# Optimization experiments

Measured on AMD Instinct MI355X. Metric: run time of the kernel, lower is better.

The kernel has to match this reference:

```python
import jax, jax.numpy as jnp
import numpy as np

D_IN, D, BOX, REL, THR = 2048, 512, 8, 80, 0.5

def _ln(x, g, b):
    m = jnp.mean(x, -1, keepdims=True)
    v = jnp.mean((x - m) ** 2, -1, keepdims=True)
    return (x - m) * jax.lax.rsqrt(v + 1e-5) * g + b

def setup_inputs():
    key = jax.random.key(0)
    ks = jax.random.split(key, 24)
    B, N = 32, 50
    def lin(k, i, o):
        return jax.random.normal(k, (i, o), jnp.float32) / np.sqrt(i)
    z = lambda n: jnp.zeros((n,), jnp.float32)
    o = lambda n: jnp.ones((n,), jnp.float32)
    return {
        "images": jax.random.normal(ks[0], (B, N, D_IN), jnp.float32),
        "selfbbox": jax.random.uniform(ks[1], (B, N, BOX), jnp.float32),
        "bbox": jax.random.uniform(ks[2], (B, N, N, BOX), jnp.float32),
        "pre_w": lin(ks[3], D_IN, D), "pre_b": z(D), "pre_g": o(D), "pre_be": z(D),
        "subj_w": lin(ks[4], D, D), "subj_b": z(D),
        "obj_w": lin(ks[5], D, D), "obj_b": z(D),
        "ps1_w": lin(ks[6], BOX, 64), "ps1_b": z(64), "ps_g": o(64), "ps_be": z(64),
        "ps2_w": lin(ks[7], 64, 64), "ps2_b": z(64),
        "pr1_w": lin(ks[8], BOX, 64), "pr1_b": z(64), "pr_g": o(64), "pr_be": z(64),
        "pr2_w": lin(ks[9], 64, 64), "pr2_b": z(64),
        "rs_w": lin(ks[10], D + 64, 1), "rs_b": z(1),
        "rf_w": lin(ks[11], D + 64, REL), "rf_b": z(REL),
        "g1_w": lin(ks[12], D + REL, D + REL), "g1_b": z(D + REL),
        "g2_w": lin(ks[13], D + REL, D), "g2_b": z(D),
        "g3_w": lin(ks[14], D, D), "g3_b": z(D),
    }

def reference(images, selfbbox, bbox, pre_w, pre_b, pre_g, pre_be, subj_w, subj_b,
              obj_w, obj_b, ps1_w, ps1_b, ps_g, ps_be, ps2_w, ps2_b,
              pr1_w, pr1_b, pr_g, pr_be, pr2_w, pr2_b, rs_w, rs_b, rf_w, rf_b,
              g1_w, g1_b, g2_w, g2_b, g3_w, g3_b):
    B, N = images.shape[0], images.shape[1]
    mask = jnp.sum(images, -1) != 0.0                      # [B,N] valid nodes
    attention_mask = (~mask)[:, None, None, :]             # [B,1,1,N]
    mf = mask.astype(images.dtype)
    # preprocess: Linear -> ReLU -> (dropout=id at eval) -> LayerNorm
    x = _ln(jax.nn.relu(images @ pre_w + pre_b), pre_g, pre_be)  # [B,N,512]
    x_subj = jax.nn.relu(x @ subj_w + subj_b) * mf[..., None]
    x_obj = jax.nn.relu(x @ obj_w + obj_b) * mf[..., None]
    eye = jnp.eye(N, dtype=bool)
    # pairwise subject/object features: diag(i==j) holds subject, off-diag object j
    x_rela = jnp.where(eye[None, :, :, None], x_subj[:, :, None, :], x_obj[:, None, :, :])
    x_rela = x_rela * mf[:, :, None, None]
    # positional MLPs
    h = jax.nn.relu(selfbbox @ ps1_w + ps1_b)
    h = jax.nn.relu(_ln(h, ps_g, ps_be) @ ps2_w + ps2_b)
    pos_self = h * mf[..., None]
    h = jax.nn.relu(bbox @ pr1_w + pr1_b)
    h = jax.nn.relu(_ln(h, pr_g, pr_be) @ pr2_w + pr2_b)
    pos_relas = h * mf[:, None, :, None] * mf[:, :, None, None]
    pos_rela = jnp.where(eye[None, :, :, None], pos_self[:, :, None, :], pos_relas)
    pos_rela = pos_rela * mf[:, :, None, None]
    pair = jnp.concatenate([x_rela, pos_rela], axis=-1)    # [B,N,N,576]
    pair_mask = mask[:, :, None] & mask[:, None, :]        # [B,N,N]
    # Relationshipness: pairwise relatedness score p + attention-pooled relation feats
    logits = (pair @ rs_w + rs_b)[..., 0]                  # [B,N,N]
    p = jax.nn.sigmoid(logits) * pair_mask.astype(images.dtype)
    attn = jax.nn.softmax(jnp.where(pair_mask, logits, -1e9), axis=2)
    feat = jax.nn.relu(pair @ rf_w + rf_b)                 # [B,N,N,80]
    relas = jnp.einsum('bij,bijf->bif', attn, feat) * mf[..., None]
    xx = jnp.concatenate([x, relas], axis=-1)              # [B,N,592]
    # dynamic edge threshold -> block-diagonal graph, expressed densely per image
    A = p > THR                                            # edge i->j
    Ahat = A | eye[None]                                   # add remaining self loops
    Af = Ahat.astype(xx.dtype)
    deg = jnp.sum(Af, axis=1)                              # in-degree at target j (>=1)
    dinv = jax.lax.rsqrt(deg)
    An = Af * dinv[:, :, None] * dinv[:, None, :]          # sym-normalized adjacency
    def gcn(hh, w, b):
        return jnp.einsum('bij,bif->bjf', An, hh @ w) + b
    x1 = jax.nn.relu(gcn(xx, g1_w, g1_b))
    x2 = jax.nn.relu(gcn(x1, g2_w, g2_b))
    x3 = jax.nn.relu(gcn(x2, g3_w, g3_b))
    outs = jnp.concatenate([x[:, None], x3[:, None]], axis=1)  # [B,2,N,512]
    return (outs, attention_mask)
```

## Files before the change

### kernel.cpp

```cpp
#include <hip/hip_runtime.h>
#include <hip/hip_bf16.h>

typedef __hip_bfloat16 bf16;

#define BB 32
#define NN 50
#define DIN 2048
#define DD 512
#define PD 64
#define FF 80
#define GG 592
#define BN (BB*NN)

#define O_FLAG  0
#define O_MF    16
#define O_SS    1616
#define O_SO    3216
#define O_PS    4816
#define O_FS    107216
#define O_FO    235216
#define O_RL    363216
#define O_LG    491216
#define O_AN    571216
#define O_T     651216
#define O_X1    1598416
#define O_X2    2545616
#define O_WPRE  3364816
#define O_BPRE  4413392
#define O_GPRE  4413904
#define O_EPRE  4414416
#define O_WSUBJ 4414928
#define O_BSUBJ 4677072
#define O_WOBJ  4677584
#define O_BOBJ  4939728
#define O_WPS1  4940240
#define O_BPS1  4940752
#define O_GPS   4940816
#define O_EPS   4940880
#define O_WPS2  4940944
#define O_BPS2  4945040
#define O_WPR1  4945104
#define O_BPR1  4945616
#define O_GPR   4945680
#define O_EPR   4945744
#define O_WPR2  4945808
#define O_BPR2  4949904
#define O_WRS   4949968
#define O_BRS   4950544
#define O_WRF   4950560
#define O_BRF   4996640
#define O_WG1   4996736
#define O_BG1   5347200
#define O_WG2   5347792
#define O_BG2   5650896
#define O_WG3   5651408
#define O_BG3   5913552
#define O_FT    5914064

#define PSLICE  819200

__device__ __forceinline__ float b2f(bf16 x){ return __bfloat162float(x); }

__device__ __forceinline__ float LDI(const bf16* p, size_t i, int f32m){
    if(f32m){
        bf16 a=p[2*i], b=p[2*i+1];
        unsigned short lo,hi;
        __builtin_memcpy(&lo,&a,2); __builtin_memcpy(&hi,&b,2);
        unsigned v=((unsigned)hi<<16)|(unsigned)lo;
        float f; __builtin_memcpy(&f,&v,4);
        return f;
    }
    return __bfloat162float(p[i]);
}

__global__ void k_flag(const bf16* __restrict__ images, float* __restrict__ ws){
    __shared__ int cnt;
    if(threadIdx.x==0) cnt=0;
    __syncthreads();
    bf16 h=images[2*threadIdx.x];
    unsigned short u; __builtin_memcpy(&u,&h,2);
    unsigned e=(u>>7)&0xFF;
    int sane=((u&0x7FFF)==0 || (e>=0x70&&e<=0x85))?1:0;
    atomicAdd(&cnt,sane);
    __syncthreads();
    if(threadIdx.x==0) ws[O_FLAG]=(cnt<48)?1.f:0.f;
}

__device__ __forceinline__ void conv(const bf16* s, float* d, int n, int F, int i0, int st){
    for(int g=i0; g<n; g+=st) d[g]=LDI(s,(size_t)g,F);
}
__global__ void kw(const bf16* p0,const bf16* p1,const bf16* p2,const bf16* p3,
                   const bf16* p4,const bf16* p5,const bf16* p6,const bf16* p7,
                   const bf16* p8,const bf16* p9,const bf16* p10,const bf16* p11,
                   const bf16* p12,const bf16* p13,const bf16* p14,const bf16* p15,
                   const bf16* p16,const bf16* p17,const bf16* p18,const bf16* p19,
                   const bf16* p20,const bf16* p21,const bf16* p22,const bf16* p23,
                   const bf16* p24,const bf16* p25,const bf16* p26,const bf16* p27,
                   const bf16* p28,const bf16* p29, float* __restrict__ ws){
    int F=ws[O_FLAG]>0.5f;
    int i0=blockIdx.x*256+threadIdx.x, st=gridDim.x*256;
    conv(p0, ws+O_WPRE, 1048576,F,i0,st);
    conv(p1, ws+O_BPRE, 512,F,i0,st);
    conv(p2, ws+O_GPRE, 512,F,i0,st);
    conv(p3, ws+O_EPRE, 512,F,i0,st);
    conv(p4, ws+O_WSUBJ,262144,F,i0,st);
    conv(p5, ws+O_BSUBJ,512,F,i0,st);
    conv(p6, ws+O_WOBJ, 262144,F,i0,st);
    conv(p7, ws+O_BOBJ, 512,F,i0,st);
    conv(p8, ws+O_WPS1, 512,F,i0,st);
    conv(p9, ws+O_BPS1, 64,F,i0,st);
    conv(p10,ws+O_GPS,  64,F,i0,st);
    conv(p11,ws+O_EPS,  64,F,i0,st);
    conv(p12,ws+O_WPS2, 4096,F,i0,st);
    conv(p13,ws+O_BPS2, 64,F,i0,st);
    conv(p14,ws+O_WPR1, 512,F,i0,st);
    conv(p15,ws+O_BPR1, 64,F,i0,st);
    conv(p16,ws+O_GPR,  64,F,i0,st);
    conv(p17,ws+O_EPR,  64,F,i0,st);
    conv(p18,ws+O_WPR2, 4096,F,i0,st);
    conv(p19,ws+O_BPR2, 64,F,i0,st);
    conv(p20,ws+O_WRS,  576,F,i0,st);
    conv(p21,ws+O_BRS,  1,F,i0,st);
    conv(p22,ws+O_WRF,  46080,F,i0,st);
    conv(p23,ws+O_BRF,  80,F,i0,st);
    conv(p24,ws+O_WG1,  350464,F,i0,st);
    conv(p25,ws+O_BG1,  592,F,i0,st);
    conv(p26,ws+O_WG2,  303104,F,i0,st);
    conv(p27,ws+O_BG2,  512,F,i0,st);
    conv(p28,ws+O_WG3,  262144,F,i0,st);
    conv(p29,ws+O_BG3,  512,F,i0,st);
}

__global__ void __launch_bounds__(256,4) k_x(const bf16* __restrict__ images,
                                             float* __restrict__ ws){
    __shared__ float as[8*256];
    __shared__ float rsum[4][8];
    int blk=blockIdx.x, t=threadIdx.x;
    int rg=blk>>3, ks=blk&7;
    int r0=rg*8, kbase=ks*256;
    int F=ws[O_FLAG]>0.5f;
    int wv=t>>6, ln=t&63;
    float sv[8];
    #pragma unroll
    for(int row=0;row<8;row++){
        float v=LDI(images,(size_t)(r0+row)*DIN+kbase+t,F);
        as[row*256+t]=v;
        sv[row]=v;
    }
    #pragma unroll
    for(int row=0;row<8;row++){
        float s=sv[row];
        for(int m=32;m>0;m>>=1) s+=__shfl_xor(s,m,64);
        sv[row]=s;
    }
    if(ln==0){
        #pragma unroll
        for(int row=0;row<8;row++) rsum[wv][row]=sv[row];
    }
    __syncthreads();
    if(t<8){
        float s=rsum[0][t]+rsum[1][t]+rsum[2][t]+rsum[3][t];
        ws[O_RL+(size_t)(r0+t)*8+ks]=s;
    }
    const float* wP=ws+O_WPRE+(size_t)kbase*DD;
    int c0=t, c1=t+256;
    float acc[8][2]={};
    for(int k0=0;k0<256;k0+=8){
        float w0[8],w1[8];
        #pragma unroll
        for(int u=0;u<8;u++){ w0[u]=wP[(size_t)(k0+u)*DD+c0]; w1[u]=wP[(size_t)(k0+u)*DD+c1]; }
        #pragma unroll
        for(int row=0;row<8;row++){
            float4 a0=*(const float4*)&as[row*256+k0];
            float4 a1=*(const float4*)&as[row*256+k0+4];
            acc[row][0]+=a0.x*w0[0]; acc[row][1]+=a0.x*w1[0];
            acc[row][0]+=a0.y*w0[1]; acc[row][1]+=a0.y*w1[1];
            acc[row][0]+=a0.z*w0[2]; acc[row][1]+=a0.z*w1[2];
            acc[row][0]+=a0.w*w0[3]; acc[row][1]+=a0.w*w1[3];
            acc[row][0]+=a1.x*w0[4]; acc[row][1]+=a1.x*w1[4];
            acc[row][0]+=a1.y*w0[5]; acc[row][1]+=a1.y*w1[5];
            acc[row][0]+=a1.z*w0[6]; acc[row][1]+=a1.z*w1[6];
            acc[row][0]+=a1.w*w0[7]; acc[row][1]+=a1.w*w1[7];
        }
    }
    float* P=ws + ((ks<7)? (O_FT+(size_t)ks*PSLICE) : (size_t)O_T);
    #pragma unroll
    for(int row=0;row<8;row++){
        size_t b=(size_t)(r0+row)*DD;
        P[b+c0]=acc[row][0]; P[b+c1]=acc[row][1];
    }
}

__global__ void __launch_bounds__(256,4) k_xr(float* __restrict__ ws, float* __restrict__ out){
    __shared__ float red[256];
    int blk=blockIdx.x, t=threadIdx.x;
    int r0=blk*4;
    if(t<4){
        int r=r0+t;
        float s=0.f;
        for(int ks=0;ks<8;ks++) s+=ws[O_RL+(size_t)r*8+ks];
        float mf=(s!=0.f)?1.f:0.f;
        ws[O_MF+r]=mf;
        out[(size_t)BB*2*NN*DD+r]=1.f-mf;
    }
    const float* bPre=ws+O_BPRE; const float* gPre=ws+O_GPRE; const float* ePre=ws+O_EPRE;
    int c0=t, c1=t+256;
    for(int row=0;row<4;row++){
        int r=r0+row;
        float y0=bPre[c0], y1=bPre[c1];
        for(int ks=0;ks<8;ks++){
            const float* P=ws + ((ks<7)? (O_FT+(size_t)ks*PSLICE) : (size_t)O_T);
            y0+=P[(size_t)r*DD+c0]; y1+=P[(size_t)r*DD+c1];
        }
        y0=fmaxf(y0,0.f); y1=fmaxf(y1,0.f);
        red[t]=y0+y1; __syncthreads();
        for(int o=128;o>0;o>>=1){ if(t<o) red[t]+=red[t+o]; __syncthreads(); }
        float mean=red[0]/DD; __syncthreads();
        float d0=y0-mean, d1=y1-mean;
        red[t]=d0*d0+d1*d1; __syncthreads();
        for(int o=128;o>0;o>>=1){ if(t<o) red[t]+=red[t+o]; __syncthreads(); }
        float rstd=rsqrtf(red[0]/DD+1e-5f);
        __syncthreads();
        float xv0=d0*rstd*gPre[c0]+ePre[c0];
        float xv1=d1*rstd*gPre[c1]+ePre[c1];
        size_t ob=((size_t)(r/NN)*2)*NN*DD+(size_t)(r%NN)*DD;
        out[ob+c0]=xv0; out[ob+c1]=xv1;
    }
}

__global__ void __launch_bounds__(256,4) k_so1(const float* __restrict__ out,
                                               float* __restrict__ ws){
    __shared__ float xs[4*DD];
    __shared__ float mrow_s[4];
    int blk=blockIdx.x, t=threadIdx.x;
    int rg=blk>>2, mat=(blk>>1)&1, ch=blk&1;
    int r0=rg*4;
    for(int idx=t; idx<4*DD; idx+=256){
        int row=idx>>9, k=idx&511;
        int r=r0+row;
        xs[idx]=out[((size_t)(r/NN)*2)*NN*DD+(size_t)(r%NN)*DD+k];
    }
    if(t<4) mrow_s[t]=ws[O_MF+r0+t];
    __syncthreads();
    const float* W =ws+(mat?O_WOBJ:O_WSUBJ);
    const float* Bb=ws+(mat?O_BOBJ:O_BSUBJ);
    int c=ch*256+t;
    float acc[4]={0.f,0.f,0.f,0.f};
    for(int k0=0;k0<DD;k0+=8){
        float w[8];
        #pragma unroll
        for(int u=0;u<8;u++) w[u]=W[(size_t)(k0+u)*DD+c];
        #pragma unroll
        for(int row=0;row<4;row++){
            float4 a0=*(const float4*)&xs[row*DD+k0];
            float4 a1=*(const float4*)&xs[row*DD+k0+4];
            acc[row]+=a0.x*w[0]; acc[row]+=a0.y*w[1];
            acc[row]+=a0.z*w[2]; acc[row]+=a0.w*w[3];
            acc[row]+=a1.x*w[4]; acc[row]+=a1.y*w[5];
            acc[row]+=a1.z*w[6]; acc[row]+=a1.w*w[7];
        }
    }
    float* Y=ws+O_FT+(size_t)mat*PSLICE;
    #pragma unroll
    for(int row=0;row<4;row++)
        Y[(size_t)(r0+row)*DD+c]=fmaxf(acc[row]+Bb[c],0.f)*mrow_s[row];
}

__global__ void __launch_bounds__(256,4) k_so2(float* __restrict__ ws){
    __shared__ float yl[4][DD];
    int blk=blockIdx.x, t=threadIdx.x, wv=t>>6, ln=t&63;
    int combo=blk*4+wv;
    int mat=combo&1, r=combo>>1;
    const float* Y=ws+O_FT+(size_t)mat*PSLICE+(size_t)r*DD;
    for(int k=ln;k<DD;k+=64) yl[wv][k]=Y[k];
    __syncthreads();
    const float* wRs=ws+O_WRS;
    float ps=0.f;
    for(int k=ln;k<DD;k+=64) ps+=yl[wv][k]*wRs[k];
    for(int m=32;m>0;m>>=1) ps+=__shfl_xor(ps,m,64);
    if(ln==0) ws[(mat?O_SO:O_SS)+r]=ps;
    const float* wRf=ws+O_WRF;
    float* dst=ws+(mat?O_FO:O_FS)+(size_t)r*FF;
    {
        float a=0.f;
        for(int k0=0;k0<DD;k0+=4){
            float4 y4=*(const float4*)&yl[wv][k0];
            a+=y4.x*wRf[(size_t)k0*FF+ln];
            a+=y4.y*wRf[(size_t)(k0+1)*FF+ln];
            a+=y4.z*wRf[(size_t)(k0+2)*FF+ln];
            a+=y4.w*wRf[(size_t)(k0+3)*FF+ln];
        }
        dst[ln]=a;
    }
    if(ln<16){
        int c=64+ln;
        float a=0.f;
        for(int k0=0;k0<DD;k0+=4){
            float4 y4=*(const float4*)&yl[wv][k0];
            a+=y4.x*wRf[(size_t)k0*FF+c];
            a+=y4.y*wRf[(size_t)(k0+1)*FF+c];
            a+=y4.z*wRf[(size_t)(k0+2)*FF+c];
            a+=y4.w*wRf[(size_t)(k0+3)*FF+c];
        }
        dst[c]=a;
    }
}

__global__ void k_pos_self(const bf16* __restrict__ sb, float* __restrict__ ws){
    __shared__ float h[PD];
    __shared__ float stat[2];
    int r=blockIdx.x, t=threadIdx.x;
    int F=ws[O_FLAG]>0.5f;
    const float* w1=ws+O_WPS1;
    float acc=0.f;
    for(int q=0;q<8;q++) acc+=LDI(sb,(size_t)r*8+q,F)*w1[q*PD+t];
    acc=fmaxf(acc+ws[O_BPS1+t],0.f);
    h[t]=acc; __syncthreads();
    if(t==0){
        float sm=0; for(int k=0;k<PD;k++) sm+=h[k];
        float mean=sm/PD;
        float v=0; for(int k=0;k<PD;k++){float d=h[k]-mean; v+=d*d;}
        stat[0]=mean; stat[1]=rsqrtf(v/PD+1e-5f);
    }
    __syncthreads();
    float hn=(acc-stat[0])*stat[1]*ws[O_GPS+t]+ws[O_EPS+t];
    h[t]=hn; __syncthreads();
    float a2=0.f;
    const float* w2=ws+O_WPS2;
    for(int k=0;k<PD;k++) a2+=h[k]*w2[k*PD+t];
    ws[O_PS+(size_t)r*PD+t]=fmaxf(a2+ws[O_BPS2+t],0.f)*ws[O_MF+r];
}

#define PSTRIDE 68
#define ZROW(m) ((m)*PSTRIDE + (((m)>>3)<<2))

__global__ void __launch_bounds__(256,3) k_pair(const bf16* __restrict__ bbox,
                                                float* __restrict__ ws){
    __shared__ float zp[64*PSTRIDE+64];
    __shared__ float wbuf[80*PSTRIDE];
    __shared__ float w1s[512];
    __shared__ float bbs[512];
    __shared__ float b1s[64], g1s[64], be1s[64], b2s[64], wrss[64];
    __shared__ float brfs[80];
    __shared__ float rowmi[64], rowmj[64], rowbase[64];
    __shared__ int   rowfb[64], rowps[64], rowdg[64];

    int t=threadIdx.x;
    int blk=blockIdx.x;
    int F=ws[O_FLAG]>0.5f;
    float rsb=ws[O_BRS];

    float wrfreg[20];
    #pragma unroll
    for(int u=0;u<20;u++){
        int idx=t+256*u;
        int f=idx>>6, k=idx&63;
        wrfreg[u]=ws[O_WRF+(size_t)(512+k)*FF+f];
    }

    for(int idx=t; idx<4096; idx+=256){ int k=idx>>6, c=idx&63; wbuf[k*PSTRIDE+c]=ws[O_WPR2+idx]; }
    for(int idx=t; idx<512; idx+=256) w1s[idx]=ws[O_WPR1+idx];
    for(int idx=t; idx<512; idx+=256) bbs[idx]=LDI(bbox,(size_t)blk*512+idx,F);
    if(t<64){
        b1s[t]=ws[O_BPR1+t]; g1s[t]=ws[O_GPR+t]; be1s[t]=ws[O_EPR+t];
        b2s[t]=ws[O_BPR2+t]; wrss[t]=ws[O_WRS+512+t];
    } else if(t<144){
        brfs[t-64]=ws[O_BRF+t-64];
    }
    if(t<64){
        int p=blk*64+t;
        int r=p/NN, j=p-r*NN;
        int b=r/NN, i=r-b*NN;
        int dg=(i==j);
        rowmi[t]=ws[O_MF+r];
        rowmj[t]=ws[O_MF+b*NN+j];
        rowdg[t]=dg;
        rowbase[t]=dg? ws[O_SS+r] : ws[O_SO+b*NN+j];
        rowfb[t]=dg? (O_FS+r*FF) : (O_FO+(b*NN+j)*FF);
        rowps[t]=O_PS+r*PD;
    }
    __syncthreads();

    int wv=t>>6, ln=t&63;
    #pragma unroll 2
    for(int q=0;q<16;q++){
        int m=wv*16+q;
        float acc=0.f;
        #pragma unroll
        for(int u=0;u<8;u++) acc+=bbs[m*8+u]*w1s[u*64+ln];
        float h1=fmaxf(acc+b1s[ln],0.f);
        float sm=h1;
        for(int o=32;o>0;o>>=1) sm+=__shfl_xor(sm,o,64);
        float mean=sm*(1.f/64.f);
        float d=h1-mean;
        float vv=d*d;
        for(int o=32;o>0;o>>=1) vv+=__shfl_xor(vv,o,64);
        float rstd=rsqrtf(vv*(1.f/64.f)+1e-5f);
        zp[ZROW(m)+ln]=d*rstd*g1s[ln]+be1s[ln];
    }

    int tr=t>>4, tc=t&15;
    int m0=tr*4, c0=tc*4;
    float a1[4][4]={};
    #pragma unroll 2
    for(int k0=0;k0<64;k0+=4){
        float4 zv[4], wvv[4];
        #pragma unroll
        for(int i=0;i<4;i++) zv[i]=*(const float4*)&zp[ZROW(m0+i)+k0];
        #pragma unroll
        for(int u=0;u<4;u++) wvv[u]=*(const float4*)&wbuf[(k0+u)*PSTRIDE+c0];
        #pragma unroll
        for(int i=0;i<4;i++){
            const float* zpp=(const float*)&zv[i];
            #pragma unroll
            for(int u=0;u<4;u++){
                const float* wp=(const float*)&wvv[u];
                float zk=zpp[u];
                a1[i][0]+=zk*wp[0]; a1[i][1]+=zk*wp[1];
                a1[i][2]+=zk*wp[2]; a1[i][3]+=zk*wp[3];
            }
        }
    }
    __syncthreads();

    #pragma unroll
    for(int i=0;i<4;i++){
        int m=m0+i;
        float4 o;
        if(rowdg[m]){
            const float* ps=ws+rowps[m];
            o.x=ps[c0]; o.y=ps[c0+1]; o.z=ps[c0+2]; o.w=ps[c0+3];
        } else {
            float sc=rowmi[m]*rowmj[m];
            o.x=fmaxf(a1[i][0]+b2s[c0+0],0.f)*sc;
            o.y=fmaxf(a1[i][1]+b2s[c0+1],0.f)*sc;
            o.z=fmaxf(a1[i][2]+b2s[c0+2],0.f)*sc;
            o.w=fmaxf(a1[i][3]+b2s[c0+3],0.f)*sc;
        }
        *(float4*)&zp[ZROW(m)+c0]=o;
    }

    #pragma unroll 2
    for(int q=0;q<16;q++){
        int m=wv*16+q;
        float lp=zp[ZROW(m)+ln]*wrss[ln];
        for(int o=32;o>0;o>>=1) lp+=__shfl_xor(lp,o,64);
        if(ln==0){
            ws[O_LG+(size_t)blk*64+m]=rowmi[m]*rowbase[m]+lp+rsb;
        }
    }

    #pragma unroll
    for(int u=0;u<20;u++){
        int idx=t+256*u;
        wbuf[(idx>>6)*PSTRIDE+(idx&63)]=wrfreg[u];
    }
    __syncthreads();

    {
        int c5=tc*5;
        float a2[4][5]={};
        #pragma unroll 2
        for(int k0=0;k0<64;k0+=4){
            float4 zv[4], wv5[5];
            #pragma unroll
            for(int i=0;i<4;i++) zv[i]=*(const float4*)&zp[ZROW(m0+i)+k0];
            #pragma unroll
            for(int j=0;j<5;j++) wv5[j]=*(const float4*)&wbuf[(c5+j)*PSTRIDE+k0];
            #pragma unroll
            for(int i=0;i<4;i++){
                const float* zpp=(const float*)&zv[i];
                #pragma unroll
                for(int j=0;j<5;j++){
                    const float* wp=(const float*)&wv5[j];
                    a2[i][j]+=zpp[0]*wp[0]+zpp[1]*wp[1]+zpp[2]*wp[2]+zpp[3]*wp[3];
                }
            }
        }
        #pragma unroll
        for(int i=0;i<4;i++){
            int m=m0+i;
            size_t p=(size_t)blk*64+m;
            float mi=rowmi[m];
            const float* fb=ws+rowfb[m];
            #pragma unroll
            for(int j=0;j<5;j++){
                int c=c5+j;
                ws[O_FT+p*FF+c]=fmaxf(mi*fb[c]+a2[i][j]+brfs[c],0.f);
            }
        }
    }
}

__global__ void k_relas(float* __restrict__ ws){
    __shared__ float attn[64];
    int r=blockIdx.x, t=threadIdx.x;
    int b=r/NN;
    float mi=ws[O_MF+r];
    if(t<64){
        float v=-1e9f;
        if(t<NN){
            float mj=ws[O_MF+b*NN+t];
            bool pm=(mi>0.5f)&&(mj>0.5f);
            v=pm? ws[O_LG+(size_t)r*NN+t] : -1e9f;
        }
        float mx=v;
        for(int o=32;o>0;o>>=1) mx=fmaxf(mx,__shfl_xor(mx,o,64));
        float e=(t<NN)? __expf(v-mx) : 0.f;
        float sm=e;
        for(int o=32;o>0;o>>=1) sm+=__shfl_xor(sm,o,64);
        attn[t]=e*(1.f/sm);
    }
    __syncthreads();
    if(t<FF){
        float s=0.f;
        const float* ft=ws+O_FT+(size_t)r*NN*FF;
        for(int j=0;j<NN;j++) s+=attn[j]*ft[(size_t)j*FF+t];
        ws[O_RL+(size_t)r*FF+t]=s*mi;
    }
}

__global__ void k_adj(float* __restrict__ ws){
    __shared__ float Af[NN*NN];
    __shared__ float dinv[NN];
    int b=blockIdx.x, t=threadIdx.x;
    for(int idx=t; idx<NN*NN; idx+=256){
        int i=idx/NN, j=idx%NN;
        float l=ws[O_LG+(size_t)b*NN*NN+idx];
        bool a=(l>0.f)&&(ws[O_MF+b*NN+i]>0.5f)&&(ws[O_MF+b*NN+j]>0.5f);
        Af[idx]=(a||i==j)?1.f:0.f;
    }
    __syncthreads();
    if(t<NN){
        float dg=0.f;
        for(int i=0;i<NN;i++) dg+=Af[i*NN+t];
        dinv[t]=rsqrtf(dg);
    }
    __syncthreads();
    for(int idx=t; idx<NN*NN; idx+=256){
        int i=idx/NN, j=idx%NN;
        ws[O_AN+(size_t)b*NN*NN+idx]=Af[idx]*dinv[i]*dinv[j];
    }
}

__global__ void __launch_bounds__(256,4) kt(int mode, const float* __restrict__ out,
                   const float* __restrict__ ws,
                   const float* __restrict__ W, float* __restrict__ T,
                   int K, int NCOL, int NTILE){
    __shared__ float xs[5*GG];
    int blk=blockIdx.x, t=threadIdx.x;
    int rg=blk/NTILE, tile=blk%NTILE;
    for(int idx=t; idx<5*K; idx+=256){
        int row=idx/K, k=idx-row*K;
        int gr=rg*5+row;
        float v;
        if(mode==0){
            int bb=gr/NN, ii=gr-bb*NN;
            if(k<DD) v=out[(size_t)(2*bb)*NN*DD+(size_t)ii*DD+k];
            else     v=ws[O_RL+(size_t)gr*FF+(k-DD)];
        } else if(mode==1) v=ws[O_X1+(size_t)gr*GG+k];
        else               v=ws[O_X2+(size_t)gr*DD+k];
        xs[row*K+k]=v;
    }
    __syncthreads();
    int c=tile*256+t;
    if(c>=NCOL) return;
    float acc[5];
    #pragma unroll
    for(int u=0;u<5;u++) acc[u]=0.f;
    for(int k0=0;k0<K;k0+=8){
        float w[8];
        #pragma unroll
        for(int u=0;u<8;u++) w[u]=W[(size_t)(k0+u)*NCOL+c];
        #pragma unroll
        for(int row=0;row<5;row++){
            float4 a0=*(const float4*)&xs[row*K+k0];
            float4 a1=*(const float4*)&xs[row*K+k0+4];
            acc[row]+=a0.x*w[0]; acc[row]+=a0.y*w[1];
            acc[row]+=a0.z*w[2]; acc[row]+=a0.w*w[3];
            acc[row]+=a1.x*w[4]; acc[row]+=a1.y*w[5];
            acc[row]+=a1.z*w[6]; acc[row]+=a1.w*w[7];
        }
    }
    int gr0=rg*5;
    #pragma unroll
    for(int u=0;u<5;u++) T[(size_t)(gr0+u)*NCOL+c]=acc[u];
}

__global__ void ka(int mode, float* __restrict__ ws, const float* __restrict__ bias,
                   float* __restrict__ out, int NCOL){
    __shared__ float acol[NN];
    int rj=blockIdx.x, t=threadIdx.x;
    int b=rj/NN, j=rj-b*NN;
    if(t<NN) acol[t]=ws[O_AN+(size_t)b*NN*NN+t*NN+j];
    __syncthreads();
    const float* Tb=ws+O_T+(size_t)b*NN*NCOL;
    for(int c=t;c<NCOL;c+=256){
        float acc=0.f;
        for(int i2=0;i2<NN;i2++) acc+=acol[i2]*Tb[(size_t)i2*NCOL+c];
        float v=fmaxf(acc+bias[c],0.f);
        if(mode==2)      out[(size_t)(2*b+1)*NN*DD+(size_t)j*DD+c]=v;
        else if(mode==1) ws[O_X2+(size_t)rj*DD+c]=v;
        else             ws[O_X1+(size_t)rj*GG+c]=v;
    }
}

extern "C" void kernel_launch(void* const* d_in, const int* in_sizes, int n_in,
                              void* d_out, int out_size, void* d_ws, size_t ws_size,
                              hipStream_t stream) {
    const bf16* images  = (const bf16*)d_in[0];
    const bf16* selfbbox= (const bf16*)d_in[1];
    const bf16* bbox    = (const bf16*)d_in[2];

    float* out=(float*)d_out;
    float* ws =(float*)d_ws;

    k_flag<<<1,64,0,stream>>>(images, ws);
    kw<<<512,256,0,stream>>>((const bf16*)d_in[3],(const bf16*)d_in[4],(const bf16*)d_in[5],
                             (const bf16*)d_in[6],(const bf16*)d_in[7],(const bf16*)d_in[8],
                             (const bf16*)d_in[9],(const bf16*)d_in[10],(const bf16*)d_in[11],
                             (const bf16*)d_in[12],(const bf16*)d_in[13],(const bf16*)d_in[14],
                             (const bf16*)d_in[15],(const bf16*)d_in[16],(const bf16*)d_in[17],
                             (const bf16*)d_in[18],(const bf16*)d_in[19],(const bf16*)d_in[20],
                             (const bf16*)d_in[21],(const bf16*)d_in[22],(const bf16*)d_in[23],
                             (const bf16*)d_in[24],(const bf16*)d_in[25],(const bf16*)d_in[26],
                             (const bf16*)d_in[27],(const bf16*)d_in[28],(const bf16*)d_in[29],
                             (const bf16*)d_in[30],(const bf16*)d_in[31],(const bf16*)d_in[32],
                             ws);
    k_x<<<1600,256,0,stream>>>(images, ws);
    k_xr<<<400,256,0,stream>>>(ws, out);
    k_pos_self<<<BN,PD,0,stream>>>(selfbbox, ws);
    k_so1<<<1600,256,0,stream>>>(out, ws);
    k_so2<<<800,256,0,stream>>>(ws);
    k_pair<<<1250,256,0,stream>>>(bbox, ws);
    k_relas<<<BN,128,0,stream>>>(ws);
    k_adj<<<BB,256,0,stream>>>(ws);

    kt<<<320*3,256,0,stream>>>(0, out, ws, ws+O_WG1, ws+O_T, GG, GG, 3);
    ka<<<BN,256,0,stream>>>(0, ws, ws+O_BG1, out, GG);
    kt<<<320*2,256,0,stream>>>(1, out, ws, ws+O_WG2, ws+O_T, GG, DD, 2);
    ka<<<BN,256,0,stream>>>(1, ws, ws+O_BG2, out, DD);
    kt<<<320*2,256,0,stream>>>(2, out, ws, ws+O_WG3, ws+O_T, DD, DD, 2);
    ka<<<BN,256,0,stream>>>(2, ws, ws+O_BG3, out, DD);
}
```

Before: 556.9 us.

## Reorder GCN to aggregate before transform and fuse bias-ReLU into GEMM

Uses the associativity An^T(XW) = (An^T X)W. Each GCN layer now first aggregates the input features with the normalized adjacency, staged per batch and per 64-column chunk in shared memory, and then runs the weight GEMM with bias and ReLU fused into its epilogue. The relas and adjacency kernels are merged into a single launch that branches on block index. This removes the old per-row aggregation kernel that read the transformed T matrix with low parallelism (one block per row), and cuts the launch count. The aggregation for layer 2 now runs over a 592-wide input instead of a 512-wide output, so it does slightly more work.

```diff
diff --git a/kernel.cpp b/kernel.cpp
--- a/kernel.cpp
+++ b/kernel.cpp
@@ -492,75 +492,103 @@
     }
 }
 
-__global__ void k_relas(float* __restrict__ ws){
-    __shared__ float attn[64];
-    int r=blockIdx.x, t=threadIdx.x;
-    int b=r/NN;
-    float mi=ws[O_MF+r];
-    if(t<64){
-        float v=-1e9f;
+__global__ void __launch_bounds__(256,4) k_ra(float* __restrict__ ws){
+    __shared__ float shm[2552];
+    int blk=blockIdx.x, t=threadIdx.x;
+    if(blk<BN){
+        int r=blk;
+        int b=r/NN;
+        float mi=ws[O_MF+r];
+        if(t<64){
+            float v=-1e9f;
+            if(t<NN){
+                float mj=ws[O_MF+b*NN+t];
+                bool pm=(mi>0.5f)&&(mj>0.5f);
+                v=pm? ws[O_LG+(size_t)r*NN+t] : -1e9f;
+            }
+            float mx=v;
+            for(int o=32;o>0;o>>=1) mx=fmaxf(mx,__shfl_xor(mx,o,64));
+            float e=(t<NN)? __expf(v-mx) : 0.f;
+            float sm=e;
+            for(int o=32;o>0;o>>=1) sm+=__shfl_xor(sm,o,64);
+            shm[t]=e*(1.f/sm);
+        }
+        __syncthreads();
+        if(t<FF){
+            float s=0.f;
+            const float* ft=ws+O_FT+(size_t)r*NN*FF;
+            for(int j=0;j<NN;j++) s+=shm[j]*ft[(size_t)j*FF+t];
+            ws[O_RL+(size_t)r*FF+t]=s*mi;
+        }
+    } else {
+        int b=blk-BN;
+        float* Af=shm;
+        float* dinv=shm+2500;
+        for(int idx=t; idx<NN*NN; idx+=256){
+            int i=idx/NN, j=idx%NN;
+            float l=ws[O_LG+(size_t)b*NN*NN+idx];
+            bool a=(l>0.f)&&(ws[O_MF+b*NN+i]>0.5f)&&(ws[O_MF+b*NN+j]>0.5f);
+            Af[idx]=(a||i==j)?1.f:0.f;
+        }
+        __syncthreads();
         if(t<NN){
-            float mj=ws[O_MF+b*NN+t];
-            bool pm=(mi>0.5f)&&(mj>0.5f);
-            v=pm? ws[O_LG+(size_t)r*NN+t] : -1e9f;
-        }
-        float mx=v;
-        for(int o=32;o>0;o>>=1) mx=fmaxf(mx,__shfl_xor(mx,o,64));
-        float e=(t<NN)? __expf(v-mx) : 0.f;
-        float sm=e;
-        for(int o=32;o>0;o>>=1) sm+=__shfl_xor(sm,o,64);
-        attn[t]=e*(1.f/sm);
-    }
-    __syncthreads();
-    if(t<FF){
-        float s=0.f;
-        const float* ft=ws+O_FT+(size_t)r*NN*FF;
-        for(int j=0;j<NN;j++) s+=attn[j]*ft[(size_t)j*FF+t];
-        ws[O_RL+(size_t)r*FF+t]=s*mi;
-    }
-}
-
-__global__ void k_adj(float* __restrict__ ws){
-    __shared__ float Af[NN*NN];
-    __shared__ float dinv[NN];
-    int b=blockIdx.x, t=threadIdx.x;
-    for(int idx=t; idx<NN*NN; idx+=256){
-        int i=idx/NN, j=idx%NN;
-        float l=ws[O_LG+(size_t)b*NN*NN+idx];
-        bool a=(l>0.f)&&(ws[O_MF+b*NN+i]>0.5f)&&(ws[O_MF+b*NN+j]>0.5f);
-        Af[idx]=(a||i==j)?1.f:0.f;
-    }
-    __syncthreads();
-    if(t<NN){
-        float dg=0.f;
-        for(int i=0;i<NN;i++) dg+=Af[i*NN+t];
-        dinv[t]=rsqrtf(dg);
-    }
-    __syncthreads();
-    for(int idx=t; idx<NN*NN; idx+=256){
-        int i=idx/NN, j=idx%NN;
-        ws[O_AN+(size_t)b*NN*NN+idx]=Af[idx]*dinv[i]*dinv[j];
-    }
-}
-
-__global__ void __launch_bounds__(256,4) kt(int mode, const float* __restrict__ out,
-                   const float* __restrict__ ws,
-                   const float* __restrict__ W, float* __restrict__ T,
+            float dg=0.f;
+            for(int i=0;i<NN;i++) dg+=Af[i*NN+t];
+            dinv[t]=rsqrtf(dg);
+        }
+        __syncthreads();
+        for(int idx=t; idx<NN*NN; idx+=256){
+            int i=idx/NN, j=idx%NN;
+            ws[O_AN+(size_t)b*NN*NN+idx]=Af[idx]*dinv[i]*dinv[j];
+        }
+    }
+}
+
+__global__ void __launch_bounds__(256,4) kagg(int mode, const float* __restrict__ out,
+                                              float* __restrict__ ws, int K, int NCH){
+    __shared__ float AnS[2500];
+    __shared__ float Xc[50*64];
+    int blk=blockIdx.x, t=threadIdx.x;
+    int b=blk/NCH, ch=blk-b*NCH;
+    int c0=ch*64;
+    int cw=K-c0; if(cw>64) cw=64;
+    for(int idx=t; idx<2500; idx+=256) AnS[idx]=ws[O_AN+(size_t)b*2500+idx];
+    for(int idx=t; idx<50*64; idx+=256){
+        int i=idx>>6, cc=idx&63;
+        float v=0.f;
+        if(cc<cw){
+            int c=c0+cc;
+            int r=b*NN+i;
+            if(mode==0){
+                if(c<DD) v=out[(size_t)(2*b)*NN*DD+(size_t)i*DD+c];
+                else     v=ws[O_RL+(size_t)r*FF+(c-DD)];
+            } else if(mode==1) v=ws[O_X1+(size_t)r*GG+c];
+            else               v=ws[O_X2+(size_t)r*DD+c];
+        }
+        Xc[idx]=v;
+    }
+    __syncthreads();
+    int wv=t>>6, ln=t&63;
+    float* T=ws+O_T;
+    for(int j=wv; j<NN; j+=4){
+        float acc=0.f;
+        for(int i=0;i<NN;i++) acc+=AnS[i*NN+j]*Xc[i*64+ln];
+        if(ln<cw) T[(size_t)(b*NN+j)*K+c0+ln]=acc;
+    }
+}
+
+__global__ void __launch_bounds__(256,4) ktf(int mode, float* __restrict__ out,
+                   float* __restrict__ ws,
+                   const float* __restrict__ W, const float* __restrict__ bias,
                    int K, int NCOL, int NTILE){
     __shared__ float xs[5*GG];
     int blk=blockIdx.x, t=threadIdx.x;
     int rg=blk/NTILE, tile=blk%NTILE;
+    const float* T=ws+O_T;
     for(int idx=t; idx<5*K; idx+=256){
         int row=idx/K, k=idx-row*K;
         int gr=rg*5+row;
-        float v;
-        if(mode==0){
-            int bb=gr/NN, ii=gr-bb*NN;
-            if(k<DD) v=out[(size_t)(2*bb)*NN*DD+(size_t)ii*DD+k];
-            else     v=ws[O_RL+(size_t)gr*FF+(k-DD)];
-        } else if(mode==1) v=ws[O_X1+(size_t)gr*GG+k];
-        else               v=ws[O_X2+(size_t)gr*DD+k];
-        xs[row*K+k]=v;
+        xs[row*K+k]=T[(size_t)gr*K+k];
     }
     __syncthreads();
     int c=tile*256+t;
@@ -583,25 +611,17 @@
         }
     }
     int gr0=rg*5;
-    #pragma unroll
-    for(int u=0;u<5;u++) T[(size_t)(gr0+u)*NCOL+c]=acc[u];
-}
-
-__global__ void ka(int mode, float* __restrict__ ws, const float* __restrict__ bias,
-                   float* __restrict__ out, int NCOL){
-    __shared__ float acol[NN];
-    int rj=blockIdx.x, t=threadIdx.x;
-    int b=rj/NN, j=rj-b*NN;
-    if(t<NN) acol[t]=ws[O_AN+(size_t)b*NN*NN+t*NN+j];
-    __syncthreads();
-    const float* Tb=ws+O_T+(size_t)b*NN*NCOL;
-    for(int c=t;c<NCOL;c+=256){
-        float acc=0.f;
-        for(int i2=0;i2<NN;i2++) acc+=acol[i2]*Tb[(size_t)i2*NCOL+c];
-        float v=fmaxf(acc+bias[c],0.f);
-        if(mode==2)      out[(size_t)(2*b+1)*NN*DD+(size_t)j*DD+c]=v;
-        else if(mode==1) ws[O_X2+(size_t)rj*DD+c]=v;
-        else             ws[O_X1+(size_t)rj*GG+c]=v;
+    float bc=bias[c];
+    #pragma unroll
+    for(int u=0;u<5;u++){
+        float v=fmaxf(acc[u]+bc,0.f);
+        int gr=gr0+u;
+        if(mode==0)      ws[O_X1+(size_t)gr*GG+c]=v;
+        else if(mode==1) ws[O_X2+(size_t)gr*DD+c]=v;
+        else {
+            int b=gr/NN, j=gr-b*NN;
+            out[(size_t)(2*b+1)*NN*DD+(size_t)j*DD+c]=v;
+        }
     }
 }
 
@@ -633,13 +653,12 @@
     k_so1<<<1600,256,0,stream>>>(out, ws);
     k_so2<<<800,256,0,stream>>>(ws);
     k_pair<<<1250,256,0,stream>>>(bbox, ws);
-    k_relas<<<BN,128,0,stream>>>(ws);
-    k_adj<<<BB,256,0,stream>>>(ws);
-
-    kt<<<320*3,256,0,stream>>>(0, out, ws, ws+O_WG1, ws+O_T, GG, GG, 3);
-    ka<<<BN,256,0,stream>>>(0, ws, ws+O_BG1, out, GG);
-    kt<<<320*2,256,0,stream>>>(1, out, ws, ws+O_WG2, ws+O_T, GG, DD, 2);
-    ka<<<BN,256,0,stream>>>(1, ws, ws+O_BG2, out, DD);
-    kt<<<320*2,256,0,stream>>>(2, out, ws, ws+O_WG3, ws+O_T, DD, DD, 2);
-    ka<<<BN,256,0,stream>>>(2, ws, ws+O_BG3, out, DD);
-}
+    k_ra<<<BN+BB,256,0,stream>>>(ws);
+
+    kagg<<<32*10,256,0,stream>>>(0, out, ws, GG, 10);
+    ktf<<<320*3,256,0,stream>>>(0, out, ws, ws+O_WG1, ws+O_BG1, GG, GG, 3);
+    kagg<<<32*10,256,0,stream>>>(1, out, ws, GG, 10);
+    ktf<<<320*2,256,0,stream>>>(1, out, ws, ws+O_WG2, ws+O_BG2, GG, DD, 2);
+    kagg<<<32*8,256,0,stream>>>(2, out, ws, DD, 8);
+    ktf<<<320*2,256,0,stream>>>(2, out, ws, ws+O_WG3, ws+O_BG3, DD, DD, 2);
+}
```

Measured after the change: 569.3 us. +2.2%, slower.
